# Kernel tuning notes

Measured on AMD Instinct MI355X. Metric: run time of the kernel, lower is better.

## Reference

```python
import jax, jax.numpy as jnp
import numpy as np

D_IN, D_MODEL = 512, 256
B, N = 2, 512


def setup_inputs() -> dict:
    key = jax.random.key(0)
    ks = jax.random.split(key, 8)
    xav_x = float(np.sqrt(2.0 / (D_IN + D_MODEL)))
    xav_p = float(np.sqrt(2.0 / (4 + D_MODEL)))
    return {
        "x": jax.random.normal(ks[0], (B, N, D_IN), dtype=jnp.float32),
        "pos": jax.random.normal(ks[1], (B, N, 4), dtype=jnp.float32),
        "attn_mask": jax.random.randint(ks[2], (B, N, N), 0, 2, dtype=jnp.int32),
        "Wx": jax.random.normal(ks[3], (D_IN, D_MODEL), dtype=jnp.float32) * xav_x,
        "bx": jnp.zeros((D_MODEL,), dtype=jnp.float32),
        "Wp": jax.random.normal(ks[4], (4, D_MODEL), dtype=jnp.float32) * xav_p,
        "bp": jnp.zeros((D_MODEL,), dtype=jnp.float32),
        "w": jax.random.normal(ks[5], (D_MODEL,), dtype=jnp.float32) * 0.05,
    }


def reference(x, pos, attn_mask, Wx, bx, Wp, bp, w):
    # projected, activated inputs: [B, N, d_model]
    h = jnp.tanh(x @ Wx + bx)
    # pairwise relative positions: [B, N, N, 4]
    rel = pos[:, :, None, :] - pos[:, None, :, :]
    # position MLP + tanh: [B, N, N, d_model]
    z = jnp.tanh(rel @ Wp + bp)
    # scores via dot with weight vector: [B, N, N]
    attn = jnp.einsum("bijd,d->bij", z, w)
    mask = attn_mask != 0
    attn = jnp.where(mask, attn, -jnp.inf)
    attn = jax.nn.softmax(attn, axis=2)
    attn = jnp.where(mask, attn, 0.0)
    # dropout is identity in eval mode
    # weighted sum: [B, N, d_model]
    output = jnp.einsum("bij,bjd->bid", attn, h)
    return (output, attn)
```

## Files before the change

### kernel.cpp

```cpp
#include <hip/hip_runtime.h>
#include <hip/hip_bf16.h>
#include <math.h>

#define BATCH   2
#define SEQ     512
#define DIN     512
#define DM      256

#define LOG2E2  2.88539008177792681f

#if __has_builtin(__builtin_amdgcn_exp2f)
#define EXP2(x) __builtin_amdgcn_exp2f(x)
#else
#define EXP2(x) exp2f(x)
#endif
#if __has_builtin(__builtin_amdgcn_rcpf)
#define RCP(x) __builtin_amdgcn_rcpf(x)
#else
#define RCP(x) (1.0f / (x))
#endif

__device__ __forceinline__ float tanh_from_scaled(float targ) {
    return fmaf(-2.0f, RCP(1.0f + EXP2(targ)), 1.0f);
}

__global__ __launch_bounds__(512) void pre_k(
    const float* __restrict__ pos,
    const float* __restrict__ Wp,
    const float* __restrict__ bp,
    float* __restrict__ EA,
    float4* __restrict__ EB4)
{
    const int tid = threadIdx.x;

    if (blockIdx.x < 128) {
        const int b  = blockIdx.x >> 6;
        const int q  = blockIdx.x & 63;
        const int d0 = 4 * q;
        const float4 p = ((const float4*)pos)[b * SEQ + tid];
        float e[4];
        #pragma unroll
        for (int i = 0; i < 4; i++) {
            const int d = d0 + i;
            const float P = fmaf(p.x, Wp[d], fmaf(p.y, Wp[DM + d],
                            fmaf(p.z, Wp[2*DM + d], p.w * Wp[3*DM + d])));
            e[i] = EXP2(-LOG2E2 * P);
        }
        EB4[((size_t)(b * 64 + q)) * SEQ + tid] = make_float4(e[0], e[1], e[2], e[3]);
        return;
    }

    const int idx = blockIdx.x - 128;
    const int r2  = __builtin_amdgcn_readfirstlane(tid >> 8);
    const int d   = tid & 255;
    const int row = idx * 2 + r2;
    const float4 p = ((const float4*)pos)[row];
    const float P = fmaf(p.x, Wp[d],
                    fmaf(p.y, Wp[DM + d],
                    fmaf(p.z, Wp[2*DM + d],
                         p.w * Wp[3*DM + d])));
    EA[(size_t)row * DM + d] = EXP2(LOG2E2 * (P + bp[d]));
}

__global__ __launch_bounds__(256) void h_k(
    const float* __restrict__ x,
    const float* __restrict__ Wx,
    const float* __restrict__ bx,
    float* __restrict__ h)
{
    __shared__ float s_xt[32][68];
    __shared__ float s_wt[64][32];

    const int tid = threadIdx.x;
    const int rt  = blockIdx.x >> 3;
    const int ct  = blockIdx.x & 7;
    const int tx  = tid & 7;
    const int ty  = tid >> 3;

    float4 acc = make_float4(0.f, 0.f, 0.f, 0.f);

    for (int ks = 0; ks < 8; ks++) {
        const int k0 = ks * 64;
        #pragma unroll
        for (int s = 0; s < 2; s++) {
            const int fidx = tid * 2 + s;
            const int r = fidx >> 4, c = fidx & 15;
            const float4 v = *(const float4*)(x + (size_t)(rt * 32 + r) * DIN + k0 + 4 * c);
            *(float4*)&s_xt[r][4 * c] = v;
        }
        #pragma unroll
        for (int s = 0; s < 2; s++) {
            const int fidx = tid * 2 + s;
            const int r = fidx >> 3, c = fidx & 7;
            *(float4*)&s_wt[r][4 * c] =
                *(const float4*)(Wx + (size_t)(k0 + r) * DM + ct * 32 + 4 * c);
        }
        __syncthreads();

        #pragma unroll 8
        for (int k = 0; k < 64; k++) {
            const float  xv = s_xt[ty][k];
            const float4 wq = *(const float4*)&s_wt[k][4 * tx];
            acc.x = fmaf(xv, wq.x, acc.x);
            acc.y = fmaf(xv, wq.y, acc.y);
            acc.z = fmaf(xv, wq.z, acc.z);
            acc.w = fmaf(xv, wq.w, acc.w);
        }
        __syncthreads();
    }

    const float4 bq = *(const float4*)(bx + ct * 32 + 4 * tx);
    float4 t;
    t.x = tanh_from_scaled(LOG2E2 * (acc.x + bq.x));
    t.y = tanh_from_scaled(LOG2E2 * (acc.y + bq.y));
    t.z = tanh_from_scaled(LOG2E2 * (acc.z + bq.z));
    t.w = tanh_from_scaled(LOG2E2 * (acc.w + bq.w));
    *(float4*)(h + (size_t)(rt * 32 + ty) * DM + ct * 32 + 4 * tx) = t;
}

__global__ __launch_bounds__(512) void attend_k(
    const int*   __restrict__ mask,
    const float* __restrict__ wv,
    const float* __restrict__ EA,
    const float4* __restrict__ EB4,
    const float* __restrict__ h,
    float* __restrict__ out,
    float* __restrict__ attn_out)
{
    const int b   = blockIdx.x >> 8;
    const int i0  = (blockIdx.x & 255) * 2;
    const int tid = threadIdx.x;
    const int l   = tid & 63;

    __shared__ float4 s_eaA[64], s_eaB[64];
    __shared__ float  s_p[2][SEQ];
    __shared__ float  s_red[2][8];
    __shared__ float  s_o[7][2][DM];

    if (tid < 64) {
        s_eaA[tid] = *(const float4*)(EA + (size_t)(b * SEQ + i0) * DM + 4 * tid);
    } else if (tid < 128) {
        s_eaB[tid - 64] = *(const float4*)(EA + (size_t)(b * SEQ + i0 + 1) * DM + 4 * (tid - 64));
    }
    __syncthreads();

    const float4* __restrict__ EBj = EB4 + (size_t)b * 64 * SEQ + tid;

    float aA = 0.f, aB = 0.f;
    #pragma unroll 8
    for (int q = 0; q < 64; q++) {
        const float4 eb = EBj[(size_t)q * SEQ];
        const float4 eA = s_eaA[q];
        const float4 eB = s_eaB[q];
        const float4 wq = *(const float4*)(wv + 4 * q);

        const float yA0 = fmaf(eA.x, eb.x, 1.0f);
        const float yA1 = fmaf(eA.y, eb.y, 1.0f);
        const float yA2 = fmaf(eA.z, eb.z, 1.0f);
        const float yA3 = fmaf(eA.w, eb.w, 1.0f);
        aA = fmaf(fmaf(wq.y, yA0, wq.x * yA1), RCP(yA0 * yA1), aA);
        aA = fmaf(fmaf(wq.w, yA2, wq.z * yA3), RCP(yA2 * yA3), aA);

        const float yB0 = fmaf(eB.x, eb.x, 1.0f);
        const float yB1 = fmaf(eB.y, eb.y, 1.0f);
        const float yB2 = fmaf(eB.z, eb.z, 1.0f);
        const float yB3 = fmaf(eB.w, eb.w, 1.0f);
        aB = fmaf(fmaf(wq.y, yB0, wq.x * yB1), RCP(yB0 * yB1), aB);
        aB = fmaf(fmaf(wq.w, yB2, wq.z * yB3), RCP(yB2 * yB3), aB);
    }

    const size_t mrowA = (size_t)b * SEQ * SEQ + (size_t)i0 * SEQ + tid;
    const int mA = mask[mrowA];
    const int mB = mask[mrowA + SEQ];
    float pA = mA ? EXP2(-LOG2E2 * aA) : 0.f;
    float pB = mB ? EXP2(-LOG2E2 * aB) : 0.f;

    float sA = pA, sB = pB;
    #pragma unroll
    for (int off = 32; off; off >>= 1) {
        sA += __shfl_xor(sA, off, 64);
        sB += __shfl_xor(sB, off, 64);
    }
    if (l == 0) { s_red[0][tid >> 6] = sA; s_red[1][tid >> 6] = sB; }
    __syncthreads();

    const float4 ra = ((const float4*)s_red[0])[0], rb = ((const float4*)s_red[0])[1];
    const float4 rc = ((const float4*)s_red[1])[0], rd = ((const float4*)s_red[1])[1];
    pA *= __fdividef(1.0f, (ra.x+ra.y+ra.z+ra.w) + (rb.x+rb.y+rb.z+rb.w));
    pB *= __fdividef(1.0f, (rc.x+rc.y+rc.z+rc.w) + (rd.x+rd.y+rd.z+rd.w));

    attn_out[mrowA]       = pA;
    attn_out[mrowA + SEQ] = pB;
    s_p[0][tid] = pA;
    s_p[1][tid] = pB;
    __syncthreads();

    const int dq = tid & 63;
    const int js = __builtin_amdgcn_readfirstlane(tid >> 6);
    const float* __restrict__ hp = h + (size_t)(b * SEQ + js * 64) * DM + 4 * dq;
    const float* __restrict__ p0 = &s_p[0][js * 64];
    const float* __restrict__ p1 = &s_p[1][js * 64];

    float4 a0 = make_float4(0,0,0,0), a1 = a0;
    #pragma unroll 4
    for (int jj = 0; jj < 16; jj++) {
        const float4 P0 = *(const float4*)(p0 + 4 * jj);
        const float4 P1 = *(const float4*)(p1 + 4 * jj);
        const float4 h0 = *(const float4*)(hp + (size_t)(4*jj + 0) * DM);
        const float4 h1 = *(const float4*)(hp + (size_t)(4*jj + 1) * DM);
        const float4 h2 = *(const float4*)(hp + (size_t)(4*jj + 2) * DM);
        const float4 h3 = *(const float4*)(hp + (size_t)(4*jj + 3) * DM);

        a0.x = fmaf(P0.x,h0.x,fmaf(P0.y,h1.x,fmaf(P0.z,h2.x,fmaf(P0.w,h3.x,a0.x))));
        a0.y = fmaf(P0.x,h0.y,fmaf(P0.y,h1.y,fmaf(P0.z,h2.y,fmaf(P0.w,h3.y,a0.y))));
        a0.z = fmaf(P0.x,h0.z,fmaf(P0.y,h1.z,fmaf(P0.z,h2.z,fmaf(P0.w,h3.z,a0.z))));
        a0.w = fmaf(P0.x,h0.w,fmaf(P0.y,h1.w,fmaf(P0.z,h2.w,fmaf(P0.w,h3.w,a0.w))));
        a1.x = fmaf(P1.x,h0.x,fmaf(P1.y,h1.x,fmaf(P1.z,h2.x,fmaf(P1.w,h3.x,a1.x))));
        a1.y = fmaf(P1.x,h0.y,fmaf(P1.y,h1.y,fmaf(P1.z,h2.y,fmaf(P1.w,h3.y,a1.y))));
        a1.z = fmaf(P1.x,h0.z,fmaf(P1.y,h1.z,fmaf(P1.z,h2.z,fmaf(P1.w,h3.z,a1.z))));
        a1.w = fmaf(P1.x,h0.w,fmaf(P1.y,h1.w,fmaf(P1.z,h2.w,fmaf(P1.w,h3.w,a1.w))));
    }

    if (js > 0) {
        *(float4*)&s_o[js - 1][0][4 * dq] = a0;
        *(float4*)&s_o[js - 1][1][4 * dq] = a1;
    }
    __syncthreads();
    if (js == 0) {
        #pragma unroll
        for (int s = 0; s < 7; s++) {
            const float4 q0 = *(const float4*)&s_o[s][0][4 * dq];
            const float4 q1 = *(const float4*)&s_o[s][1][4 * dq];
            a0.x += q0.x; a0.y += q0.y; a0.z += q0.z; a0.w += q0.w;
            a1.x += q1.x; a1.y += q1.y; a1.z += q1.z; a1.w += q1.w;
        }
        float* __restrict__ op = out + (size_t)(b * SEQ + i0) * DM + 4 * dq;
        *(float4*)(op)      = a0;
        *(float4*)(op + DM) = a1;
    }
}

extern "C" void kernel_launch(void* const* d_in, const int* in_sizes, int n_in,
                              void* d_out, int out_size, void* d_ws, size_t ws_size,
                              hipStream_t stream) {
    const float* x    = (const float*)d_in[0];
    const float* pos  = (const float*)d_in[1];
    const int*   mask = (const int*)  d_in[2];
    const float* Wx   = (const float*)d_in[3];
    const float* bx   = (const float*)d_in[4];
    const float* Wp   = (const float*)d_in[5];
    const float* bp   = (const float*)d_in[6];
    const float* wv   = (const float*)d_in[7];

    float* out      = (float*)d_out;
    float* attn_out = (float*)d_out + (size_t)BATCH*SEQ*DM;

    char*   ws  = (char*)d_ws;
    float*  h   = (float*)(ws);
    float*  EA  = (float*)(ws + (size_t)BATCH*SEQ*DM*4);
    float4* EB4 = (float4*)(ws + 2*(size_t)BATCH*SEQ*DM*4);

    pre_k   <<<128 + (BATCH*SEQ)/2, 512, 0, stream>>>(pos, Wp, bp, EA, EB4);
    h_k     <<<256, 256, 0, stream>>>(x, Wx, bx, h);
    attend_k<<<(BATCH*SEQ)/2, 512, 0, stream>>>(mask, wv, EA, EB4, h, out, attn_out);
}
```

Measured before the change: 114.4 us.

## Merge h projection into producer kernel and compute EA inside attend

Folds the x@Wx tanh projection into the same launch as the EB exponent table, so blocks 0-127 build EB4 and blocks 128-255 compute h with wider 64-column tiles and 512 threads. The EA row exponentials are no longer written to workspace. Each attend block now recomputes them directly from pos and Wp into shared memory. This drops one kernel launch and the EA global round trip, at the cost of a small amount of redundant per-block arithmetic and fewer, larger GEMM blocks.

```diff
diff --git a/kernel.cpp b/kernel.cpp
--- a/kernel.cpp
+++ b/kernel.cpp
@@ -24,12 +24,14 @@
     return fmaf(-2.0f, RCP(1.0f + EXP2(targ)), 1.0f);
 }
 
-__global__ __launch_bounds__(512) void pre_k(
+__global__ __launch_bounds__(512) void produce_k(
     const float* __restrict__ pos,
     const float* __restrict__ Wp,
-    const float* __restrict__ bp,
-    float* __restrict__ EA,
-    float4* __restrict__ EB4)
+    const float* __restrict__ x,
+    const float* __restrict__ Wx,
+    const float* __restrict__ bx,
+    float4* __restrict__ EB4,
+    float* __restrict__ h)
 {
     const int tid = threadIdx.x;
 
@@ -50,50 +52,32 @@
         return;
     }
 
+    __shared__ float s_xt[32][68];
+    __shared__ float s_wt[64][64];
+
     const int idx = blockIdx.x - 128;
-    const int r2  = __builtin_amdgcn_readfirstlane(tid >> 8);
-    const int d   = tid & 255;
-    const int row = idx * 2 + r2;
-    const float4 p = ((const float4*)pos)[row];
-    const float P = fmaf(p.x, Wp[d],
-                    fmaf(p.y, Wp[DM + d],
-                    fmaf(p.z, Wp[2*DM + d],
-                         p.w * Wp[3*DM + d])));
-    EA[(size_t)row * DM + d] = EXP2(LOG2E2 * (P + bp[d]));
-}
-
-__global__ __launch_bounds__(256) void h_k(
-    const float* __restrict__ x,
-    const float* __restrict__ Wx,
-    const float* __restrict__ bx,
-    float* __restrict__ h)
-{
-    __shared__ float s_xt[32][68];
-    __shared__ float s_wt[64][32];
-
-    const int tid = threadIdx.x;
-    const int rt  = blockIdx.x >> 3;
-    const int ct  = blockIdx.x & 7;
-    const int tx  = tid & 7;
-    const int ty  = tid >> 3;
+    const int rt  = idx >> 2;
+    const int ct  = idx & 3;
+    const int ty  = tid >> 4;
+    const int tx  = tid & 15;
+    const int row = rt * 32 + ty;
+    const int dcol = ct * 64 + 4 * tx;
 
     float4 acc = make_float4(0.f, 0.f, 0.f, 0.f);
 
     for (int ks = 0; ks < 8; ks++) {
         const int k0 = ks * 64;
+        {
+            const int r = tid >> 4, c = tid & 15;
+            *(float4*)&s_xt[r][4 * c] =
+                *(const float4*)(x + (size_t)(rt * 32 + r) * DIN + k0 + 4 * c);
+        }
         #pragma unroll
         for (int s = 0; s < 2; s++) {
-            const int fidx = tid * 2 + s;
+            const int fidx = s * 512 + tid;
             const int r = fidx >> 4, c = fidx & 15;
-            const float4 v = *(const float4*)(x + (size_t)(rt * 32 + r) * DIN + k0 + 4 * c);
-            *(float4*)&s_xt[r][4 * c] = v;
-        }
-        #pragma unroll
-        for (int s = 0; s < 2; s++) {
-            const int fidx = tid * 2 + s;
-            const int r = fidx >> 3, c = fidx & 7;
             *(float4*)&s_wt[r][4 * c] =
-                *(const float4*)(Wx + (size_t)(k0 + r) * DM + ct * 32 + 4 * c);
+                *(const float4*)(Wx + (size_t)(k0 + r) * DM + ct * 64 + 4 * c);
         }
         __syncthreads();
 
@@ -109,19 +93,21 @@
         __syncthreads();
     }
 
-    const float4 bq = *(const float4*)(bx + ct * 32 + 4 * tx);
+    const float4 bq = *(const float4*)(bx + dcol);
     float4 t;
     t.x = tanh_from_scaled(LOG2E2 * (acc.x + bq.x));
     t.y = tanh_from_scaled(LOG2E2 * (acc.y + bq.y));
     t.z = tanh_from_scaled(LOG2E2 * (acc.z + bq.z));
     t.w = tanh_from_scaled(LOG2E2 * (acc.w + bq.w));
-    *(float4*)(h + (size_t)(rt * 32 + ty) * DM + ct * 32 + 4 * tx) = t;
+    *(float4*)(h + (size_t)row * DM + dcol) = t;
 }
 
 __global__ __launch_bounds__(512) void attend_k(
+    const float* __restrict__ pos,
+    const float* __restrict__ Wp,
+    const float* __restrict__ bp,
     const int*   __restrict__ mask,
     const float* __restrict__ wv,
-    const float* __restrict__ EA,
     const float4* __restrict__ EB4,
     const float* __restrict__ h,
     float* __restrict__ out,
@@ -137,10 +123,16 @@
     __shared__ float  s_red[2][8];
     __shared__ float  s_o[7][2][DM];
 
-    if (tid < 64) {
-        s_eaA[tid] = *(const float4*)(EA + (size_t)(b * SEQ + i0) * DM + 4 * tid);
-    } else if (tid < 128) {
-        s_eaB[tid - 64] = *(const float4*)(EA + (size_t)(b * SEQ + i0 + 1) * DM + 4 * (tid - 64));
+    {
+        const int rr = __builtin_amdgcn_readfirstlane(tid >> 8);
+        const int d  = tid & 255;
+        const float4 p = ((const float4*)pos)[b * SEQ + i0 + rr];
+        const float P = fmaf(p.x, Wp[d],
+                        fmaf(p.y, Wp[DM + d],
+                        fmaf(p.z, Wp[2*DM + d],
+                             p.w * Wp[3*DM + d])));
+        const float ea = EXP2(LOG2E2 * (P + bp[d]));
+        ((float*)(rr ? s_eaB : s_eaA))[d] = ea;
     }
     __syncthreads();
 
@@ -257,10 +249,8 @@
 
     char*   ws  = (char*)d_ws;
     float*  h   = (float*)(ws);
-    float*  EA  = (float*)(ws + (size_t)BATCH*SEQ*DM*4);
-    float4* EB4 = (float4*)(ws + 2*(size_t)BATCH*SEQ*DM*4);
-
-    pre_k   <<<128 + (BATCH*SEQ)/2, 512, 0, stream>>>(pos, Wp, bp, EA, EB4);
-    h_k     <<<256, 256, 0, stream>>>(x, Wx, bx, h);
-    attend_k<<<(BATCH*SEQ)/2, 512, 0, stream>>>(mask, wv, EA, EB4, h, out, attn_out);
-}
+    float4* EB4 = (float4*)(ws + (size_t)BATCH*SEQ*DM*4);
+
+    produce_k<<<256, 512, 0, stream>>>(pos, Wp, x, Wx, bx, EB4, h);
+    attend_k <<<(BATCH*SEQ)/2, 512, 0, stream>>>(pos, Wp, bp, mask, wv, EB4, h, out, attn_out);
+}
```

After: 114.8 us. No clear change (+0.3%).
